# Performance work log

Measured on AMD Instinct MI355X. Metric: run time of the kernel, lower is better.

Reference implementation:

```python
import jax, jax.numpy as jnp
import numpy as np

EPS_MSG = 1e-7   # GENConv message eps
EPS_SM = 1e-16   # scatter_softmax denom eps
EPS_BN = 1e-5    # BatchNorm1d eps


def genconv(x, src, dst, t, W1, W2, gamma, beta):
    """One GENConv (aggr='softmax', learn_t, edge_attr=None, bias=False)."""
    n = x.shape[0]
    # message: relu(x_j) + eps over edges  [E, d]
    msg = jax.nn.relu(x[src]) + EPS_MSG
    # softmax over edges sharing a destination, per feature, temperature t
    logits = msg * t
    m = jax.ops.segment_max(logits, dst, num_segments=n)
    m = jnp.where(jnp.isfinite(m), m, 0.0)          # empty segments -> 0
    w = jnp.exp(logits - m[dst])
    denom = jax.ops.segment_sum(w, dst, num_segments=n) + EPS_SM
    aggr = jax.ops.segment_sum(w * msg, dst, num_segments=n) / denom
    # update: MLP(aggr + x); MLP = Lin(d,2d) -> BN -> ReLU -> Lin(2d,d)
    h = aggr + x
    h1 = h @ W1
    mean = jnp.mean(h1, axis=0)
    var = jnp.var(h1, axis=0)
    h1 = (h1 - mean) * jax.lax.rsqrt(var + EPS_BN) * gamma + beta
    h1 = jax.nn.relu(h1)
    return h1 @ W2


def setup_inputs() -> dict:
    key = jax.random.key(0)
    ks = jax.random.split(key, 4)
    N, E, D = 100000, 800000, 128
    x = jax.random.normal(ks[0], (N, D), dtype=jnp.float32)
    edge_index = jax.random.randint(ks[1], (2, E), 0, N, dtype=jnp.int64)
    t_all = jnp.ones((4,), dtype=jnp.float32)  # learn_t init 1.0
    W1_all = jax.random.normal(ks[2], (4, D, 2 * D), dtype=jnp.float32) * (1.0 / np.sqrt(D))
    W2_all = jax.random.normal(ks[3], (4, 2 * D, D), dtype=jnp.float32) * (1.0 / np.sqrt(2 * D))
    gamma_all = jnp.ones((4, 2 * D), dtype=jnp.float32)
    beta_all = jnp.zeros((4, 2 * D), dtype=jnp.float32)
    return {"x": x, "edge_index": edge_index, "t_all": t_all,
            "W1_all": W1_all, "W2_all": W2_all,
            "gamma_all": gamma_all, "beta_all": beta_all}


def reference(x, edge_index, t_all, W1_all, W2_all, gamma_all, beta_all):
    src, dst = edge_index[0], edge_index[1]
    n_aggr = 2
    h = x
    for i in range(n_aggr):
        h = genconv(h, src, dst, t_all[i], W1_all[i], W2_all[i], gamma_all[i], beta_all[i])
        h = jax.nn.relu(h)
        # dropout: identity (inference)
    mu = genconv(h, src, dst, t_all[2], W1_all[2], W2_all[2], gamma_all[2], beta_all[2])
    logstd = genconv(h, src, dst, t_all[3], W1_all[3], W2_all[3], gamma_all[3], beta_all[3])
    return (mu, logstd)
```

## Files before the change

kernel.cpp:

```cpp
#include <hip/hip_runtime.h>
#include <math.h>

#define D 128
#define H 256

typedef short s16x8 __attribute__((ext_vector_type(8)));
typedef float f32x4 __attribute__((ext_vector_type(4)));
typedef unsigned short u16;
typedef unsigned int u32;

__device__ __forceinline__ u16 f2b(float f) {
    union { float f; unsigned u; } c;
    c.f = f;
    unsigned u = c.u + 0x7FFFu + ((c.u >> 16) & 1u);
    return (u16)(u >> 16);
}
__device__ __forceinline__ float b2f(u16 h) {
    union { unsigned u; float f; } c;
    c.u = ((unsigned)h) << 16;
    return c.f;
}
__device__ __forceinline__ float blo(u32 p) {
    union { unsigned u; float f; } c;
    c.u = p << 16;
    return c.f;
}
__device__ __forceinline__ float bhi(u32 p) {
    union { unsigned u; float f; } c;
    c.u = p & 0xFFFF0000u;
    return c.f;
}


__global__ __launch_bounds__(256) void k_count(const int* __restrict__ dstA,
                                               int* __restrict__ deg, int E) {
    int e = blockIdx.x * 256 + threadIdx.x;
    if (e < E) atomicAdd(&deg[dstA[e]], 1);
}

__global__ __launch_bounds__(1024) void k_scan1(const int* __restrict__ deg,
                                                int* __restrict__ rowptr,
                                                int* __restrict__ bsum, int N) {
    __shared__ int tmp[1024];
    int t = threadIdx.x;
    int i = blockIdx.x * 1024 + t;
    int v = (i < N) ? deg[i] : 0;
    tmp[t] = v;
    __syncthreads();
    #pragma unroll
    for (int off = 1; off < 1024; off <<= 1) {
        int u = (t >= off) ? tmp[t - off] : 0;
        __syncthreads();
        tmp[t] += u;
        __syncthreads();
    }
    if (i < N) rowptr[i] = tmp[t] - v;
    if (t == 1023) bsum[blockIdx.x] = tmp[1023];
}

__global__ __launch_bounds__(1024) void k_scan2(int* __restrict__ bsum, int B) {
    __shared__ int sums[1024];
    int t = threadIdx.x;
    int chunk = (B + 1023) >> 10;
    int beg = t * chunk;
    int end = beg + chunk;
    if (end > B) end = B;
    int s = 0;
    for (int i = beg; i < end; ++i) s += bsum[i];
    sums[t] = s;
    __syncthreads();
    #pragma unroll
    for (int off = 1; off < 1024; off <<= 1) {
        int v = (t >= off) ? sums[t - off] : 0;
        __syncthreads();
        sums[t] += v;
        __syncthreads();
    }
    int run = (t == 0) ? 0 : sums[t - 1];
    for (int i = beg; i < end; ++i) {
        int v = bsum[i];
        bsum[i] = run;
        run += v;
    }
}

__global__ __launch_bounds__(1024) void k_scan3(int* __restrict__ rowptr,
                                                const int* __restrict__ bsum,
                                                int N, int E) {
    int i = blockIdx.x * 1024 + threadIdx.x;
    if (i < N) rowptr[i] += bsum[blockIdx.x];
    else if (i == N) rowptr[N] = E;
}

__global__ __launch_bounds__(256) void k_scatter(const int* __restrict__ srcA,
                                                 const int* __restrict__ dstA,
                                                 const int* __restrict__ rowptr,
                                                 int* __restrict__ cnt,
                                                 int* __restrict__ srcs, int E) {
    int e = blockIdx.x * 256 + threadIdx.x;
    if (e < E) {
        int d = dstA[e];
        int p = rowptr[d] + atomicAdd(&cnt[d], 1);
        srcs[p] = srcA[e];
    }
}


__global__ __launch_bounds__(256) void k_cvt(const float* __restrict__ x,
                                             u16* __restrict__ xb, int n4) {
    int i = blockIdx.x * 256 + threadIdx.x;
    if (i < n4) {
        float4 v = ((const float4*)x)[i];
        xb[i * 4 + 0] = f2b(v.x);
        xb[i * 4 + 1] = f2b(v.y);
        xb[i * 4 + 2] = f2b(v.z);
        xb[i * 4 + 3] = f2b(v.w);
    }
}

__global__ __launch_bounds__(256) void k_prep(const float* __restrict__ W1_all,
                                              const float* __restrict__ W2_all,
                                              u16* __restrict__ WT1,
                                              u16* __restrict__ WT2) {
    int id = blockIdx.x * 256 + threadIdx.x;
    if (id < 131072) {
        int l = id >> 15, rem = id & 32767, n = rem >> 7, k = rem & 127;
        WT1[id] = f2b(W1_all[l * 32768 + k * 256 + n]);
    } else {
        int id2 = id - 131072;
        int l = id2 >> 15, rem = id2 & 32767, n = rem >> 8, k = rem & 255;
        WT2[id2] = f2b(W2_all[l * 32768 + k * 128 + n]);
    }
}


__global__ __launch_bounds__(256) void k_edge(const u16* __restrict__ hin,
                                              const int* __restrict__ rowptr,
                                              const int* __restrict__ srcs,
                                              const float* __restrict__ tptr,
                                              u16* __restrict__ g,
                                              float* __restrict__ bnsum,
                                              float* __restrict__ bnss, int N) {
    if (blockIdx.x == 0) {
        bnsum[threadIdx.x] = 0.f;
        bnss[threadIdx.x] = 0.f;
    }
    int u = blockIdx.x * 4 + (threadIdx.x >> 6);
    if (u >= N) return;
    u = __builtin_amdgcn_readfirstlane(u);
    int lane = threadIdx.x & 63;
    const u32* hin32 = (const u32*)hin;
    float t = *tptr;
    int beg = rowptr[u], end = rowptr[u + 1];
    int cnt = end - beg;

    u32 pu = hin32[(size_t)u * 64 + lane];

    float s0 = 0.f, s1 = 0.f, sn0 = 0.f, sn1 = 0.f;
    float mx = -3.0e38f, mv = 0.f;

    for (int b = 0; b < cnt; b += 64) {
        int nb = cnt - b;
        if (nb > 64) nb = 64;
        int sv = (b + lane < cnt) ? srcs[beg + b + lane] : 0;
        for (int ib = 0; ib < nb; ib += 16) {
            int m = nb - ib;
            if (m > 16) m = 16;
            u32 pr[16];
            #pragma unroll
            for (int j = 0; j < 16; ++j) {
                if (j < m) {
                    int vi = __builtin_amdgcn_readlane(sv, ib + j);
                    pr[j] = hin32[(size_t)vi * 64 + lane];
                }
            }
            #pragma unroll
            for (int j = 0; j < 16; ++j) {
                if (j < m) {
                    u32 p = pr[j];
                    float v0 = fmaxf(blo(p), 0.f) + 1e-7f;
                    float v1 = fmaxf(bhi(p), 0.f) + 1e-7f;
                    float l0 = v0 * t, l1 = v1 * t;
                    mx = fmaxf(mx, fmaxf(l0, l1));
                    mv = fmaxf(mv, fmaxf(v0, v1));
                    float w0 = __expf(l0), w1 = __expf(l1);
                    s0 += w0; s1 += w1;
                    sn0 = fmaf(w0, v0, sn0);
                    sn1 = fmaf(w1, v1, sn1);
                }
            }
        }
    }

    bool has = (cnt > 0);
    if (__any(has && (mx > 60.f || mx < -20.f || mv > 1.0e10f))) {
        float m0 = -3.0e38f, m1 = -3.0e38f;
        s0 = s1 = sn0 = sn1 = 0.f;
        for (int e = beg; e < end; ++e) {
            int v = srcs[e];
            u32 p = hin32[(size_t)v * 64 + lane];
            float v0 = fmaxf(blo(p), 0.f) + 1e-7f;
            float v1 = fmaxf(bhi(p), 0.f) + 1e-7f;
            float l0 = v0 * t, l1 = v1 * t;
            float nm0 = fmaxf(m0, l0), nm1 = fmaxf(m1, l1);
            float a0 = __expf(m0 - nm0), a1 = __expf(m1 - nm1);
            float w0 = __expf(l0 - nm0), w1 = __expf(l1 - nm1);
            s0 = s0 * a0 + w0;           s1 = s1 * a1 + w1;
            sn0 = sn0 * a0 + w0 * v0;    sn1 = sn1 * a1 + w1 * v1;
            m0 = nm0; m1 = nm1;
        }
    }

    float aggr0 = sn0 / (s0 + 1e-16f);
    float aggr1 = sn1 / (s1 + 1e-16f);
    float o0 = aggr0 + blo(pu);
    float o1 = aggr1 + bhi(pu);
    ((u32*)g)[(size_t)u * 64 + lane] = (u32)f2b(o0) | ((u32)f2b(o1) << 16);
}


__global__ __launch_bounds__(256) void k_mm1(const u16* __restrict__ A,
                                             const u16* __restrict__ WT,
                                             u16* __restrict__ C,
                                             float* __restrict__ bnsum,
                                             float* __restrict__ bnss, int M) {
    __shared__ u16 As[128][72];
    __shared__ u16 Bs[128][72];
    __shared__ float csum[128], css[128];
    int row0 = blockIdx.x * 128, n0 = blockIdx.y * 128;
    int tid = threadIdx.x;
    int lane = tid & 63, w = tid >> 6;
    int r0w = (w & 1) * 64, c0w = (w >> 1) * 64;
    int q = lane >> 4, ml = lane & 15;

    if (tid < 128) { csum[tid] = 0.f; css[tid] = 0.f; }

    f32x4 acc[4][4];
    #pragma unroll
    for (int i = 0; i < 4; ++i)
        #pragma unroll
        for (int j = 0; j < 4; ++j) acc[i][j] = f32x4{0.f, 0.f, 0.f, 0.f};

    for (int kk = 0; kk < 128; kk += 64) {
        #pragma unroll
        for (int i = 0; i < 4; ++i) {
            int r = i * 32 + (tid >> 3);
            int c8 = (tid & 7) * 8;
            s16x8 va = s16x8{0, 0, 0, 0, 0, 0, 0, 0};
            if (row0 + r < M)
                va = *reinterpret_cast<const s16x8*>(&A[(size_t)(row0 + r) * 128 + kk + c8]);
            *reinterpret_cast<s16x8*>(&As[r][c8]) = va;
            s16x8 vb = *reinterpret_cast<const s16x8*>(&WT[(size_t)(n0 + r) * 128 + kk + c8]);
            *reinterpret_cast<s16x8*>(&Bs[r][c8]) = vb;
        }
        __syncthreads();
        #pragma unroll
        for (int ks = 0; ks < 64; ks += 32) {
            s16x8 af[4], bfr[4];
            #pragma unroll
            for (int rt = 0; rt < 4; ++rt)
                af[rt] = *reinterpret_cast<const s16x8*>(&As[r0w + rt * 16 + ml][ks + q * 8]);
            #pragma unroll
            for (int ct = 0; ct < 4; ++ct)
                bfr[ct] = *reinterpret_cast<const s16x8*>(&Bs[c0w + ct * 16 + ml][ks + q * 8]);
            #pragma unroll
            for (int rt = 0; rt < 4; ++rt)
                #pragma unroll
                for (int ct = 0; ct < 4; ++ct)
                    acc[rt][ct] = __builtin_amdgcn_mfma_f32_16x16x32_bf16(
                        af[rt], bfr[ct], acc[rt][ct], 0, 0, 0);
        }
        __syncthreads();
    }

    #pragma unroll
    for (int ct = 0; ct < 4; ++ct) {
        float s = 0.f, ss = 0.f;
        int col = n0 + c0w + ct * 16 + ml;
        #pragma unroll
        for (int rt = 0; rt < 4; ++rt) {
            int rbase = row0 + r0w + rt * 16 + q * 4;
            #pragma unroll
            for (int rg = 0; rg < 4; ++rg) {
                float v = acc[rt][ct][rg];
                s += v;
                ss += v * v;
                if (rbase + rg < M)
                    C[(size_t)(rbase + rg) * H + col] = f2b(v);
            }
        }
        atomicAdd(&csum[c0w + ct * 16 + ml], s);
        atomicAdd(&css[c0w + ct * 16 + ml], ss);
    }
    __syncthreads();
    if (tid < 128) {
        atomicAdd(&bnsum[n0 + tid], csum[tid]);
        atomicAdd(&bnss[n0 + tid], css[tid]);
    }
}


__global__ __launch_bounds__(256) void k_bnfin(const float* __restrict__ bnsum,
                                               const float* __restrict__ bnss,
                                               const float* __restrict__ gamma,
                                               const float* __restrict__ beta,
                                               float* __restrict__ scale,
                                               float* __restrict__ shift, int M) {
    int c = threadIdx.x;
    float inv = 1.0f / (float)M;
    float mean = bnsum[c] * inv;
    float var = bnss[c] * inv - mean * mean;
    if (var < 0.f) var = 0.f;
    float rstd = rsqrtf(var + 1e-5f);
    float sc = rstd * gamma[c];
    scale[c] = sc;
    shift[c] = beta[c] - mean * sc;
}


__global__ __launch_bounds__(256) void k_mm2(const u16* __restrict__ H1,
                                             const float* __restrict__ scale,
                                             const float* __restrict__ shift,
                                             const u16* __restrict__ WT,
                                             float* __restrict__ outf,
                                             u16* __restrict__ outb, int M) {
    __shared__ u16 As[128][72];
    __shared__ u16 Bs[128][72];
    int row0 = blockIdx.x * 128;
    int tid = threadIdx.x;
    int lane = tid & 63, w = tid >> 6;
    int r0w = (w & 1) * 64, c0w = (w >> 1) * 64;
    int q = lane >> 4, ml = lane & 15;

    f32x4 acc[4][4];
    #pragma unroll
    for (int i = 0; i < 4; ++i)
        #pragma unroll
        for (int j = 0; j < 4; ++j) acc[i][j] = f32x4{0.f, 0.f, 0.f, 0.f};

    for (int kk = 0; kk < 256; kk += 64) {
        #pragma unroll
        for (int i = 0; i < 4; ++i) {
            int r = i * 32 + (tid >> 3);
            int c8 = (tid & 7) * 8;
            s16x8 o = s16x8{0, 0, 0, 0, 0, 0, 0, 0};
            if (row0 + r < M) {
                s16x8 v = *reinterpret_cast<const s16x8*>(&H1[(size_t)(row0 + r) * H + kk + c8]);
                #pragma unroll
                for (int j = 0; j < 8; ++j) {
                    float f = b2f((u16)v[j]) * scale[kk + c8 + j] + shift[kk + c8 + j];
                    o[j] = (short)f2b(fmaxf(f, 0.f));
                }
            }
            *reinterpret_cast<s16x8*>(&As[r][c8]) = o;
            s16x8 vb = *reinterpret_cast<const s16x8*>(&WT[(size_t)r * H + kk + c8]);
            *reinterpret_cast<s16x8*>(&Bs[r][c8]) = vb;
        }
        __syncthreads();
        #pragma unroll
        for (int ks = 0; ks < 64; ks += 32) {
            s16x8 af[4], bfr[4];
            #pragma unroll
            for (int rt = 0; rt < 4; ++rt)
                af[rt] = *reinterpret_cast<const s16x8*>(&As[r0w + rt * 16 + ml][ks + q * 8]);
            #pragma unroll
            for (int ct = 0; ct < 4; ++ct)
                bfr[ct] = *reinterpret_cast<const s16x8*>(&Bs[c0w + ct * 16 + ml][ks + q * 8]);
            #pragma unroll
            for (int rt = 0; rt < 4; ++rt)
                #pragma unroll
                for (int ct = 0; ct < 4; ++ct)
                    acc[rt][ct] = __builtin_amdgcn_mfma_f32_16x16x32_bf16(
                        af[rt], bfr[ct], acc[rt][ct], 0, 0, 0);
        }
        __syncthreads();
    }

    #pragma unroll
    for (int ct = 0; ct < 4; ++ct) {
        int col = c0w + ct * 16 + ml;
        #pragma unroll
        for (int rt = 0; rt < 4; ++rt) {
            int rbase = row0 + r0w + rt * 16 + q * 4;
            #pragma unroll
            for (int rg = 0; rg < 4; ++rg) {
                if (rbase + rg < M) {
                    float v = acc[rt][ct][rg];
                    if (outb)
                        outb[(size_t)(rbase + rg) * D + col] = f2b(fmaxf(v, 0.f));
                    else
                        outf[(size_t)(rbase + rg) * D + col] = v;
                }
            }
        }
    }
}


extern "C" void kernel_launch(void* const* d_in, const int* in_sizes, int n_in,
                              void* d_out, int out_size, void* d_ws, size_t ws_size,
                              hipStream_t stream) {
    const float* x         = (const float*)d_in[0];
    const int*   ei        = (const int*)d_in[1];
    const float* t_all     = (const float*)d_in[2];
    const float* W1_all    = (const float*)d_in[3];
    const float* W2_all    = (const float*)d_in[4];
    const float* gamma_all = (const float*)d_in[5];
    const float* beta_all  = (const float*)d_in[6];

    int N = in_sizes[0] / D;
    int E = in_sizes[1] / 2;
    float* out = (float*)d_out;

    char* ws = (char*)d_ws;
    size_t off = 0;
    auto alloc = [&](size_t bytes) -> void* {
        void* p = ws + off;
        off += (bytes + 255) & ~(size_t)255;
        return p;
    };
    int B = (N + 1023) >> 10;
    int* rowptr = (int*)alloc((size_t)(N + 1) * 4);
    int* deg    = (int*)alloc((size_t)N * 4);
    int* srcs   = (int*)alloc((size_t)E * 4);
    int* bsum   = (int*)alloc((size_t)(B + 1) * 4);
    u16* xb     = (u16*)alloc((size_t)N * D * 2);
    u16* a0     = (u16*)alloc((size_t)N * D * 2);
    u16* a1     = (u16*)alloc((size_t)N * D * 2);
    u16* g      = (u16*)alloc((size_t)N * D * 2);
    u16* h1     = (u16*)alloc((size_t)N * H * 2);
    u16* WT1    = (u16*)alloc((size_t)4 * H * D * 2);
    u16* WT2    = (u16*)alloc((size_t)4 * D * H * 2);
    float* bnsum = (float*)alloc(H * 4);
    float* bnss  = (float*)alloc(H * 4);
    float* scale = (float*)alloc(H * 4);
    float* shift = (float*)alloc(H * 4);
    (void)ws_size; (void)n_in; (void)out_size;

    const int* srcA = ei;
    const int* dstA = ei + E;

    k_cvt<<<(N * D / 4 + 255) / 256, 256, 0, stream>>>(x, xb, N * D / 4);
    k_prep<<<1024, 256, 0, stream>>>(W1_all, W2_all, WT1, WT2);

    hipMemsetAsync(deg, 0, (size_t)N * 4, stream);
    k_count<<<(E + 255) / 256, 256, 0, stream>>>(dstA, deg, E);
    k_scan1<<<B, 1024, 0, stream>>>(deg, rowptr, bsum, N);
    k_scan2<<<1, 1024, 0, stream>>>(bsum, B);
    k_scan3<<<(N + 1 + 1023) / 1024, 1024, 0, stream>>>(rowptr, bsum, N, E);
    hipMemsetAsync(deg, 0, (size_t)N * 4, stream);
    k_scatter<<<(E + 255) / 256, 256, 0, stream>>>(srcA, dstA, rowptr, deg, srcs, E);

    float* out0 = out;
    float* out1 = out + (size_t)N * D;

    int gx = (N + 127) / 128;
    for (int layer = 0; layer < 4; ++layer) {
        const u16* hin = (layer == 0) ? xb : (layer == 1 ? a0 : a1);
        k_edge<<<(N + 3) / 4, 256, 0, stream>>>(hin, rowptr, srcs, t_all + layer,
                                                g, bnsum, bnss, N);

        k_mm1<<<dim3(gx, 2), 256, 0, stream>>>(g, WT1 + (size_t)layer * H * D, h1,
                                               bnsum, bnss, N);
        k_bnfin<<<1, H, 0, stream>>>(bnsum, bnss, gamma_all + (size_t)layer * H,
                                     beta_all + (size_t)layer * H, scale, shift, N);

        float* outf = nullptr;
        u16*   outb = nullptr;
        if (layer == 0)      outb = a0;
        else if (layer == 1) outb = a1;
        else if (layer == 2) outf = out0;
        else                 outf = out1;

        k_mm2<<<dim3(gx, 1), 256, 0, stream>>>(h1, scale, shift,
                                               WT2 + (size_t)layer * D * H,
                                               outf, outb, N);
    }
}
```

Before: 932.8 us.

## Transpose MFMA operands for vectorized stores and slot-split BN stat atomics

Swaps the MFMA operand order so each lane holds four consecutive columns of one row, which lets the GEMM epilogues write packed 8-byte bf16 or 16-byte fp32 stores instead of scalar 2/4-byte scattered stores. The BatchNorm column statistics are now reduced with wave shuffles instead of shared-memory atomics. The global atomics are spread over 64 slot copies to reduce contention, and the finalize kernel sums the slots. The cost is a slightly longer finalize loop and extra zeroing in the edge kernel.

```diff
diff --git a/kernel.cpp b/kernel.cpp
--- a/kernel.cpp
+++ b/kernel.cpp
@@ -3,9 +3,11 @@
 
 #define D 128
 #define H 256
+#define NSLOT 64
 
 typedef short s16x8 __attribute__((ext_vector_type(8)));
 typedef float f32x4 __attribute__((ext_vector_type(4)));
+typedef unsigned int u32x2 __attribute__((ext_vector_type(2)));
 typedef unsigned short u16;
 typedef unsigned int u32;
 
@@ -139,11 +141,11 @@
                                               const int* __restrict__ srcs,
                                               const float* __restrict__ tptr,
                                               u16* __restrict__ g,
-                                              float* __restrict__ bnsum,
-                                              float* __restrict__ bnss, int N) {
-    if (blockIdx.x == 0) {
-        bnsum[threadIdx.x] = 0.f;
-        bnss[threadIdx.x] = 0.f;
+                                              float* __restrict__ psum,
+                                              float* __restrict__ pss, int N) {
+    if (blockIdx.x < NSLOT) {
+        psum[blockIdx.x * 256 + threadIdx.x] = 0.f;
+        pss[blockIdx.x * 256 + threadIdx.x] = 0.f;
     }
     int u = blockIdx.x * 4 + (threadIdx.x >> 6);
     if (u >= N) return;
@@ -222,18 +224,16 @@
 __global__ __launch_bounds__(256) void k_mm1(const u16* __restrict__ A,
                                              const u16* __restrict__ WT,
                                              u16* __restrict__ C,
-                                             float* __restrict__ bnsum,
-                                             float* __restrict__ bnss, int M) {
+                                             float* __restrict__ psum,
+                                             float* __restrict__ pss, int M) {
     __shared__ u16 As[128][72];
     __shared__ u16 Bs[128][72];
-    __shared__ float csum[128], css[128];
+    __shared__ float csumA[128], cssA[128], csumB[128], cssB[128];
     int row0 = blockIdx.x * 128, n0 = blockIdx.y * 128;
     int tid = threadIdx.x;
     int lane = tid & 63, w = tid >> 6;
     int r0w = (w & 1) * 64, c0w = (w >> 1) * 64;
     int q = lane >> 4, ml = lane & 15;
-
-    if (tid < 128) { csum[tid] = 0.f; css[tid] = 0.f; }
 
     f32x4 acc[4][4];
     #pragma unroll
@@ -268,48 +268,86 @@
                 #pragma unroll
                 for (int ct = 0; ct < 4; ++ct)
                     acc[rt][ct] = __builtin_amdgcn_mfma_f32_16x16x32_bf16(
-                        af[rt], bfr[ct], acc[rt][ct], 0, 0, 0);
-        }
-        __syncthreads();
-    }
-
-    #pragma unroll
-    for (int ct = 0; ct < 4; ++ct) {
-        float s = 0.f, ss = 0.f;
-        int col = n0 + c0w + ct * 16 + ml;
-        #pragma unroll
-        for (int rt = 0; rt < 4; ++rt) {
-            int rbase = row0 + r0w + rt * 16 + q * 4;
-            #pragma unroll
-            for (int rg = 0; rg < 4; ++rg) {
-                float v = acc[rt][ct][rg];
+                        bfr[ct], af[rt], acc[rt][ct], 0, 0, 0);
+        }
+        __syncthreads();
+    }
+
+    #pragma unroll
+    for (int rt = 0; rt < 4; ++rt) {
+        int row = row0 + r0w + rt * 16 + ml;
+        if (row < M) {
+            #pragma unroll
+            for (int ct = 0; ct < 4; ++ct) {
+                f32x4 a = acc[rt][ct];
+                u32x2 p;
+                p.x = (u32)f2b(a[0]) | ((u32)f2b(a[1]) << 16);
+                p.y = (u32)f2b(a[2]) | ((u32)f2b(a[3]) << 16);
+                int col = n0 + c0w + ct * 16 + q * 4;
+                *reinterpret_cast<u32x2*>(&C[(size_t)row * H + col]) = p;
+            }
+        }
+    }
+
+    float sp[16], ssp[16];
+    #pragma unroll
+    for (int ct = 0; ct < 4; ++ct)
+        #pragma unroll
+        for (int r = 0; r < 4; ++r) {
+            float s = 0.f, ss = 0.f;
+            #pragma unroll
+            for (int rt = 0; rt < 4; ++rt) {
+                float v = acc[rt][ct][r];
                 s += v;
                 ss += v * v;
-                if (rbase + rg < M)
-                    C[(size_t)(rbase + rg) * H + col] = f2b(v);
-            }
-        }
-        atomicAdd(&csum[c0w + ct * 16 + ml], s);
-        atomicAdd(&css[c0w + ct * 16 + ml], ss);
+            }
+            sp[ct * 4 + r] = s;
+            ssp[ct * 4 + r] = ss;
+        }
+    #pragma unroll
+    for (int msk = 1; msk < 16; msk <<= 1) {
+        #pragma unroll
+        for (int i = 0; i < 16; ++i) {
+            sp[i] += __shfl_xor(sp[i], msk);
+            ssp[i] += __shfl_xor(ssp[i], msk);
+        }
+    }
+    if (ml == 0) {
+        float* cs = (w & 1) ? csumB : csumA;
+        float* cq = (w & 1) ? cssB : cssA;
+        #pragma unroll
+        for (int ct = 0; ct < 4; ++ct)
+            #pragma unroll
+            for (int r = 0; r < 4; ++r) {
+                int col = c0w + ct * 16 + q * 4 + r;
+                cs[col] = sp[ct * 4 + r];
+                cq[col] = ssp[ct * 4 + r];
+            }
     }
     __syncthreads();
     if (tid < 128) {
-        atomicAdd(&bnsum[n0 + tid], csum[tid]);
-        atomicAdd(&bnss[n0 + tid], css[tid]);
-    }
-}
-
-
-__global__ __launch_bounds__(256) void k_bnfin(const float* __restrict__ bnsum,
-                                               const float* __restrict__ bnss,
+        int slot = blockIdx.x & (NSLOT - 1);
+        atomicAdd(&psum[(size_t)slot * 256 + n0 + tid], csumA[tid] + csumB[tid]);
+        atomicAdd(&pss[(size_t)slot * 256 + n0 + tid], cssA[tid] + cssB[tid]);
+    }
+}
+
+
+__global__ __launch_bounds__(256) void k_bnfin(const float* __restrict__ psum,
+                                               const float* __restrict__ pss,
                                                const float* __restrict__ gamma,
                                                const float* __restrict__ beta,
                                                float* __restrict__ scale,
                                                float* __restrict__ shift, int M) {
     int c = threadIdx.x;
+    float s = 0.f, ss = 0.f;
+    for (int b = 0; b < NSLOT; ++b) {
+        s += psum[b * 256 + c];
+        ss += pss[b * 256 + c];
+    }
     float inv = 1.0f / (float)M;
-    float mean = bnsum[c] * inv;
-    float var = bnss[c] * inv - mean * mean;
+    float mean = s * inv;
+    float var = ss * inv - mean * mean;
     if (var < 0.f) var = 0.f;
     float rstd = rsqrtf(var + 1e-5f);
     float sc = rstd * gamma[c];
@@ -371,25 +409,26 @@
                 #pragma unroll
                 for (int ct = 0; ct < 4; ++ct)
                     acc[rt][ct] = __builtin_amdgcn_mfma_f32_16x16x32_bf16(
-                        af[rt], bfr[ct], acc[rt][ct], 0, 0, 0);
-        }
-        __syncthreads();
-    }
-
-    #pragma unroll
-    for (int ct = 0; ct < 4; ++ct) {
-        int col = c0w + ct * 16 + ml;
-        #pragma unroll
-        for (int rt = 0; rt < 4; ++rt) {
-            int rbase = row0 + r0w + rt * 16 + q * 4;
-            #pragma unroll
-            for (int rg = 0; rg < 4; ++rg) {
-                if (rbase + rg < M) {
-                    float v = acc[rt][ct][rg];
-                    if (outb)
-                        outb[(size_t)(rbase + rg) * D + col] = f2b(fmaxf(v, 0.f));
-                    else
-                        outf[(size_t)(rbase + rg) * D + col] = v;
+                        bfr[ct], af[rt], acc[rt][ct], 0, 0, 0);
+        }
+        __syncthreads();
+    }
+
+    #pragma unroll
+    for (int rt = 0; rt < 4; ++rt) {
+        int row = row0 + r0w + rt * 16 + ml;
+        if (row < M) {
+            #pragma unroll
+            for (int ct = 0; ct < 4; ++ct) {
+                f32x4 a = acc[rt][ct];
+                int col = c0w + ct * 16 + q * 4;
+                if (outb) {
+                    u32x2 p;
+                    p.x = (u32)f2b(fmaxf(a[0], 0.f)) | ((u32)f2b(fmaxf(a[1], 0.f)) << 16);
+                    p.y = (u32)f2b(fmaxf(a[2], 0.f)) | ((u32)f2b(fmaxf(a[3], 0.f)) << 16);
+                    *reinterpret_cast<u32x2*>(&outb[(size_t)row * D + col]) = p;
+                } else {
+                    *reinterpret_cast<f32x4*>(&outf[(size_t)row * D + col]) = a;
                 }
             }
         }
@@ -431,8 +470,8 @@
     u16* h1     = (u16*)alloc((size_t)N * H * 2);
     u16* WT1    = (u16*)alloc((size_t)4 * H * D * 2);
     u16* WT2    = (u16*)alloc((size_t)4 * D * H * 2);
-    float* bnsum = (float*)alloc(H * 4);
-    float* bnss  = (float*)alloc(H * 4);
+    float* psum = (float*)alloc((size_t)NSLOT * 256 * 4);
+    float* pss  = (float*)alloc((size_t)NSLOT * 256 * 4);
     float* scale = (float*)alloc(H * 4);
     float* shift = (float*)alloc(H * 4);
     (void)ws_size; (void)n_in; (void)out_size;
@@ -458,11 +497,11 @@
     for (int layer = 0; layer < 4; ++layer) {
         const u16* hin = (layer == 0) ? xb : (layer == 1 ? a0 : a1);
         k_edge<<<(N + 3) / 4, 256, 0, stream>>>(hin, rowptr, srcs, t_all + layer,
-                                                g, bnsum, bnss, N);
+                                                g, psum, pss, N);
 
         k_mm1<<<dim3(gx, 2), 256, 0, stream>>>(g, WT1 + (size_t)layer * H * D, h1,
-                                               bnsum, bnss, N);
-        k_bnfin<<<1, H, 0, stream>>>(bnsum, bnss, gamma_all + (size_t)layer * H,
+                                               psum, pss, N);
+        k_bnfin<<<1, H, 0, stream>>>(psum, pss, gamma_all + (size_t)layer * H,
                                      beta_all + (size_t)layer * H, scale, shift, N);
 
         float* outf = nullptr;
```

New measurement: 800.1 us. 1.17x faster.
